# Kernel tuning notes

Measured on AMD Instinct MI355X. Metric: run time of the kernel, lower is better.

Reference implementation:

```python
import jax, jax.numpy as jnp
import numpy as np

N_NODES = 100000
N_EDGES = 3200000
N_GRAPHS = 1000
C = 11   # atomic features
D = 4    # bond features
BN_EPS = 1e-5


def setup_inputs() -> dict:
    key = jax.random.key(0)
    ks = jax.random.split(key, 20)
    inp = {
        "x": jax.random.normal(ks[0], (N_NODES, C), dtype=jnp.float32),
        "edge_index": jax.random.randint(ks[1], (2, N_EDGES), 0, N_NODES),
        "edge_attr": jax.random.uniform(ks[2], (N_EDGES, D), dtype=jnp.float32),
        "batch": jnp.sort(jax.random.randint(ks[3], (N_NODES,), 0, N_GRAPHS)),
    }
    s = 0.3
    # CGConv layer 1 params: lin_f, lin_s take z=[x_i, x_j, e] of dim 2C+D
    inp["Wf1"] = jax.random.normal(ks[4], (2 * C + D, C), dtype=jnp.float32) * s
    inp["bf1"] = jnp.zeros((C,), jnp.float32)
    inp["Ws1"] = jax.random.normal(ks[5], (2 * C + D, C), dtype=jnp.float32) * s
    inp["bs1"] = jnp.zeros((C,), jnp.float32)
    inp["gamma1"] = jnp.ones((C,), jnp.float32)
    inp["beta1"] = jnp.zeros((C,), jnp.float32)
    # CGConv layer 2
    inp["Wf2"] = jax.random.normal(ks[6], (2 * C + D, C), dtype=jnp.float32) * s
    inp["bf2"] = jnp.zeros((C,), jnp.float32)
    inp["Ws2"] = jax.random.normal(ks[7], (2 * C + D, C), dtype=jnp.float32) * s
    inp["bs2"] = jnp.zeros((C,), jnp.float32)
    inp["gamma2"] = jnp.ones((C,), jnp.float32)
    inp["beta2"] = jnp.zeros((C,), jnp.float32)
    # MLP head
    inp["W_fc1"] = jax.random.normal(ks[8], (C, 5), dtype=jnp.float32) * s
    inp["b_fc1"] = jnp.zeros((5,), jnp.float32)
    inp["W_fc2"] = jax.random.normal(ks[9], (5, 1), dtype=jnp.float32) * s
    inp["b_fc2"] = jnp.zeros((1,), jnp.float32)
    return inp


def _cgconv(x, src, dst, e, Wf, bf, Ws, bs, gamma, beta):
    # z = [x_i, x_j, e_ij] per edge; message = sigmoid(lin_f(z)) * softplus(lin_s(z))
    z = jnp.concatenate([x[dst], x[src], e], axis=-1)          # [E, 2C+D]
    msg = jax.nn.sigmoid(z @ Wf + bf) * jax.nn.softplus(z @ Ws + bs)  # [E, C]
    agg = jax.ops.segment_sum(msg, dst, num_segments=N_NODES)  # [N, C]
    # BatchNorm1d (training-mode: batch statistics over nodes)
    mu = jnp.mean(agg, axis=0)
    var = jnp.var(agg, axis=0)
    agg = (agg - mu) * jax.lax.rsqrt(var + BN_EPS) * gamma + beta
    return x + agg  # residual


def reference(x, edge_index, edge_attr, batch,
              Wf1, bf1, Ws1, bs1, gamma1, beta1,
              Wf2, bf2, Ws2, bs2, gamma2, beta2,
              W_fc1, b_fc1, W_fc2, b_fc2):
    src, dst = edge_index[0], edge_index[1]
    h = _cgconv(x, src, dst, edge_attr, Wf1, bf1, Ws1, bs1, gamma1, beta1)
    h = _cgconv(h, src, dst, edge_attr, Wf2, bf2, Ws2, bs2, gamma2, beta2)
    # global mean pool per graph
    sums = jax.ops.segment_sum(h, batch, num_segments=N_GRAPHS)        # [G, C]
    cnts = jax.ops.segment_sum(jnp.ones((h.shape[0],), h.dtype), batch,
                               num_segments=N_GRAPHS)
    pooled = sums / jnp.maximum(cnts, 1.0)[:, None]
    out = jax.nn.softplus(pooled @ W_fc1 + b_fc1)
    out = out @ W_fc2 + b_fc2                                          # [G, 1]
    return out
```

## Files before the change

### kernel.cpp

```cpp
#include <hip/hip_runtime.h>
#include <math.h>

#define N_NODES 100000
#define N_EDGES 3200000
#define N_GRAPHS 1000
#define C 11
#define D 4
#define AST 12
#define XWST 24
#define BN_EPS 1e-5f
#define LOG2E 1.44269504088896f
#define LN2   0.69314718055994f
#define QSCALE (1.0f/65535.0f)

#define BSHIFT 8
#define BNODES 256
#define NB ((N_NODES + BNODES - 1) / BNODES)
#define CAP 8704
#define EPB 8192
#define PBLK ((N_EDGES + EPB - 1) / EPB)
#define SB 64
#define PST 48

__device__ __forceinline__ float fast_sigmoid(float x) {
    float e = exp2f(-LOG2E * x);
    return __builtin_amdgcn_rcpf(1.0f + e);
}
__device__ __forceinline__ float fast_softplus(float x) {
    float e = exp2f(LOG2E * x);
    float l = log2f(1.0f + e) * LN2;
    return (x > 20.0f) ? x : l;
}

__global__ void __launch_bounds__(256) partition_kernel(
    const int* __restrict__ ei, const float4* __restrict__ ea,
    int* __restrict__ bcur, uint3* __restrict__ grp)
{
    __shared__ int lh[NB];
    __shared__ int lbase[NB];
    for (int i = threadIdx.x; i < NB; i += 256) lh[i] = 0;
    __syncthreads();
    int e0 = blockIdx.x * EPB;
    for (int r = 0; r < EPB; r += 256) {
        int e = e0 + r + threadIdx.x;
        if (e < N_EDGES) atomicAdd(&lh[ei[N_EDGES + e] >> BSHIFT], 1);
    }
    __syncthreads();
    for (int b = threadIdx.x; b < NB; b += 256) {
        lbase[b] = atomicAdd(&bcur[b], lh[b]);
        lh[b] = 0;
    }
    __syncthreads();
    for (int r = 0; r < EPB; r += 256) {
        int e = e0 + r + threadIdx.x;
        if (e < N_EDGES) {
            int d = ei[N_EDGES + e];
            int s = ei[e];
            float4 v = ea[e];
            unsigned q0 = (unsigned)(v.x * 65535.0f + 0.5f);
            unsigned q1 = (unsigned)(v.y * 65535.0f + 0.5f);
            unsigned q2 = (unsigned)(v.z * 65535.0f + 0.5f);
            unsigned q3 = (unsigned)(v.w * 65535.0f + 0.5f);
            int b = d >> BSHIFT;
            int ofs = lbase[b] + atomicAdd(&lh[b], 1);
            grp[(size_t)b * CAP + ofs] =
                make_uint3((unsigned)s | ((unsigned)(d & 255) << 17),
                           q0 | (q1 << 16), q2 | (q3 << 16));
        }
    }
}

__global__ void __launch_bounds__(512) bscan_kernel(
    const int* __restrict__ bcur, int* __restrict__ bexcl, int* __restrict__ off)
{
    __shared__ int wsum[8];
    int t = threadIdx.x;
    int lane = t & 63, w = t >> 6;
    int v = (t < NB) ? bcur[t] : 0;
    int incl = v;
    #pragma unroll
    for (int d = 1; d < 64; d <<= 1) {
        int u = __shfl_up(incl, d);
        if (lane >= d) incl += u;
    }
    if (lane == 63) wsum[w] = incl;
    __syncthreads();
    if (w == 0) {
        int x = (lane < 8) ? wsum[lane] : 0;
        #pragma unroll
        for (int d = 1; d < 8; d <<= 1) {
            int u = __shfl_up(x, d);
            if (lane >= d) x += u;
        }
        if (lane < 8) wsum[lane] = x;
    }
    __syncthreads();
    int excl = incl - v + (w > 0 ? wsum[w - 1] : 0);
    if (t < NB) bexcl[t] = excl;
    if (t == 0) { bexcl[NB] = N_EDGES; off[N_NODES] = N_EDGES; }
}

__global__ void __launch_bounds__(256) finalize_kernel(
    const uint3* __restrict__ grp, const int* __restrict__ bcur,
    const int* __restrict__ bexcl,
    int* __restrict__ off, uint3* __restrict__ rec)
{
    __shared__ int lcnt[BNODES];
    __shared__ int lexcl[BNODES];
    __shared__ int wsum[4];
    int b = blockIdx.x;
    int cnt = min(bcur[b], CAP);
    int base = bexcl[b];
    const uint3* g = grp + (size_t)b * CAP;
    int t = threadIdx.x;
    lcnt[t] = 0;
    __syncthreads();
    for (int i = t; i < cnt; i += 256)
        atomicAdd(&lcnt[(g[i].x >> 17) & 255], 1);
    __syncthreads();
    int lane = t & 63, w = t >> 6;
    int v = lcnt[t];
    int incl = v;
    #pragma unroll
    for (int d = 1; d < 64; d <<= 1) {
        int u = __shfl_up(incl, d);
        if (lane >= d) incl += u;
    }
    if (lane == 63) wsum[w] = incl;
    __syncthreads();
    if (w == 0) {
        int x = (lane < 4) ? wsum[lane] : 0;
        #pragma unroll
        for (int d = 1; d < 4; d <<= 1) {
            int u = __shfl_up(x, d);
            if (lane >= d) x += u;
        }
        if (lane < 4) wsum[lane] = x;
    }
    __syncthreads();
    int excl = incl - v + (w > 0 ? wsum[w - 1] : 0);
    lexcl[t] = excl;
    int n = (b << BSHIFT) + t;
    if (n < N_NODES) off[n] = base + excl;
    lcnt[t] = 0;
    __syncthreads();
    for (int i = t; i < cnt; i += 256) {
        uint3 r = g[i];
        int nl = (r.x >> 17) & 255;
        int pos = base + lexcl[nl] + atomicAdd(&lcnt[nl], 1);
        rec[pos] = make_uint3(r.x & 0x1FFFFu, r.y, r.z);
    }
}

__global__ void __launch_bounds__(256) pre_kernel(
    const float* __restrict__ xin, int stride,
    const float* __restrict__ Wf, const float* __restrict__ Ws,
    const float* __restrict__ bf, const float* __restrict__ bs,
    float* __restrict__ xwd, float* __restrict__ xws)
{
    __shared__ float sW[22 * C * 2];
    __shared__ float sbf[C], sbs[C];
    for (int i = threadIdx.x; i < 22 * C; i += blockDim.x) {
        sW[2 * i] = Wf[i];
        sW[2 * i + 1] = Ws[i];
    }
    if (threadIdx.x < C) { sbf[threadIdx.x] = bf[threadIdx.x]; sbs[threadIdx.x] = bs[threadIdx.x]; }
    __syncthreads();

    int n = blockIdx.x * blockDim.x + threadIdx.x;
    if (n >= N_NODES) return;
    float xi[C];
    #pragma unroll
    for (int j = 0; j < C; ++j) xi[j] = xin[n * stride + j];

    float od[XWST], os[XWST];
    #pragma unroll
    for (int c = 0; c < C; ++c) {
        float f = sbf[c], s = sbs[c];
        float f2 = 0.0f, s2 = 0.0f;
        #pragma unroll
        for (int j = 0; j < C; ++j) {
            f  = fmaf(xi[j], sW[2 * (j * C + c)], f);
            s  = fmaf(xi[j], sW[2 * (j * C + c) + 1], s);
            f2 = fmaf(xi[j], sW[2 * ((C + j) * C + c)], f2);
            s2 = fmaf(xi[j], sW[2 * ((C + j) * C + c) + 1], s2);
        }
        od[2 * c] = f; od[2 * c + 1] = s;
        os[2 * c] = f2; os[2 * c + 1] = s2;
    }
    od[22] = 0.0f; od[23] = 0.0f; os[22] = 0.0f; os[23] = 0.0f;
    float4* pd = (float4*)(xwd + (size_t)n * XWST);
    float4* ps = (float4*)(xws + (size_t)n * XWST);
    #pragma unroll
    for (int i = 0; i < 6; ++i) {
        pd[i] = make_float4(od[4 * i], od[4 * i + 1], od[4 * i + 2], od[4 * i + 3]);
        ps[i] = make_float4(os[4 * i], os[4 * i + 1], os[4 * i + 2], os[4 * i + 3]);
    }
}

__global__ void __launch_bounds__(256) conv_kernel(
    const uint3* __restrict__ rec, const int* __restrict__ off,
    const float* __restrict__ xwd, const float* __restrict__ xws,
    const float* __restrict__ Wf, const float* __restrict__ Ws,
    float* __restrict__ agg)
{
    int tid = blockIdx.x * blockDim.x + threadIdx.x;
    int n = tid >> 3;
    int t = tid & 7;
    if (n >= N_NODES) return;

    float weaf[44], weas[44];
    {
        const float2* pf = (const float2*)(Wf + 22 * C);
        const float2* ps = (const float2*)(Ws + 22 * C);
        #pragma unroll
        for (int i = 0; i < 22; ++i) {
            float2 a = pf[i], b = ps[i];
            weaf[2 * i] = a.x; weaf[2 * i + 1] = a.y;
            weas[2 * i] = b.x; weas[2 * i + 1] = b.y;
        }
    }
    float based[XWST];
    {
        const float4* pd = (const float4*)(xwd + (size_t)n * XWST);
        #pragma unroll
        for (int i = 0; i < 6; ++i) {
            float4 a = pd[i];
            based[4 * i] = a.x; based[4 * i + 1] = a.y;
            based[4 * i + 2] = a.z; based[4 * i + 3] = a.w;
        }
    }

    float acc[C];
    #pragma unroll
    for (int c = 0; c < C; ++c) acc[c] = 0.0f;

    int e1 = off[n + 1];
    for (int k = off[n] + t; k < e1; k += 8) {
        uint3 r = rec[k];
        int src = (int)r.x;
        float ea0 = (float)(r.y & 0xFFFFu) * QSCALE;
        float ea1 = (float)(r.y >> 16) * QSCALE;
        float ea2 = (float)(r.z & 0xFFFFu) * QSCALE;
        float ea3 = (float)(r.z >> 16) * QSCALE;
        float xsr[XWST];
        {
            const float4* px = (const float4*)(xws + (size_t)src * XWST);
            #pragma unroll
            for (int i = 0; i < 6; ++i) {
                float4 a = px[i];
                xsr[4 * i] = a.x; xsr[4 * i + 1] = a.y;
                xsr[4 * i + 2] = a.z; xsr[4 * i + 3] = a.w;
            }
        }
        #pragma unroll
        for (int c = 0; c < C; ++c) {
            float f = based[2 * c] + xsr[2 * c];
            float s = based[2 * c + 1] + xsr[2 * c + 1];
            f = fmaf(ea0, weaf[c], f);         s = fmaf(ea0, weas[c], s);
            f = fmaf(ea1, weaf[C + c], f);     s = fmaf(ea1, weas[C + c], s);
            f = fmaf(ea2, weaf[2 * C + c], f); s = fmaf(ea2, weas[2 * C + c], s);
            f = fmaf(ea3, weaf[3 * C + c], f); s = fmaf(ea3, weas[3 * C + c], s);
            acc[c] += fast_sigmoid(f) * fast_softplus(s);
        }
    }

    #pragma unroll
    for (int c = 0; c < C; ++c) {
        acc[c] += __shfl_xor(acc[c], 1);
        acc[c] += __shfl_xor(acc[c], 2);
        acc[c] += __shfl_xor(acc[c], 4);
    }
    if (t == 0) {
        float4* pa = (float4*)(agg + (size_t)n * AST);
        pa[0] = make_float4(acc[0], acc[1], acc[2], acc[3]);
        pa[1] = make_float4(acc[4], acc[5], acc[6], acc[7]);
        pa[2] = make_float4(acc[8], acc[9], acc[10], 0.0f);
    }
}

__global__ void __launch_bounds__(256) bn_stats_kernel(
    const float* __restrict__ agg, float* __restrict__ pstats )
{
    float s[C], q[C];
    #pragma unroll
    for (int c = 0; c < C; ++c) { s[c] = 0.0f; q[c] = 0.0f; }
    for (int n = blockIdx.x * 256 + threadIdx.x; n < N_NODES; n += SB * 256) {
        const float4* pa = (const float4*)(agg + (size_t)n * AST);
        float4 a0 = pa[0], a1 = pa[1], a2 = pa[2];
        float v[C] = {a0.x, a0.y, a0.z, a0.w, a1.x, a1.y, a1.z, a1.w,
                      a2.x, a2.y, a2.z};
        #pragma unroll
        for (int c = 0; c < C; ++c) { s[c] += v[c]; q[c] += v[c] * v[c]; }
    }
    #pragma unroll
    for (int c = 0; c < C; ++c) {
        #pragma unroll
        for (int o = 32; o > 0; o >>= 1) {
            s[c] += __shfl_down(s[c], o);
            q[c] += __shfl_down(q[c], o);
        }
    }
    __shared__ float ls[2 * C + 2];
    if (threadIdx.x < 2 * C + 2) ls[threadIdx.x] = 0.0f;
    __syncthreads();
    if ((threadIdx.x & 63) == 0) {
        #pragma unroll
        for (int c = 0; c < C; ++c) {
            atomicAdd(&ls[2 * c], s[c]);
            atomicAdd(&ls[2 * c + 1], q[c]);
        }
    }
    __syncthreads();
    if (threadIdx.x < 2 * C)
        pstats[blockIdx.x * PST + threadIdx.x] = ls[threadIdx.x];
}

__device__ __forceinline__ void reduce_stats(
    const float* __restrict__ pstats, float* smu, float* srs)
{
    if (threadIdx.x < C) {
        double sum = 0.0, sq = 0.0;
        for (int b = 0; b < SB; ++b) {
            sum += (double)pstats[b * PST + 2 * threadIdx.x];
            sq  += (double)pstats[b * PST + 2 * threadIdx.x + 1];
        }
        double mu = sum / (double)N_NODES;
        double var = sq / (double)N_NODES - mu * mu;
        smu[threadIdx.x] = (float)mu;
        srs[threadIdx.x] = (float)(1.0 / sqrt(var + (double)BN_EPS));
    }
}

__global__ void __launch_bounds__(256) bnpre_kernel(
    const float* __restrict__ xin, const float* __restrict__ agg,
    const float* __restrict__ pstats,
    const float* __restrict__ gamma, const float* __restrict__ beta,
    const float* __restrict__ Wf, const float* __restrict__ Ws,
    const float* __restrict__ bf, const float* __restrict__ bs,
    float* __restrict__ hout, float* __restrict__ xwd, float* __restrict__ xws)
{
    __shared__ float sW[22 * C * 2];
    __shared__ float sbf[C], sbs[C];
    __shared__ float smu[C], srs[C], sg[C], sb[C];
    for (int i = threadIdx.x; i < 22 * C; i += blockDim.x) {
        sW[2 * i] = Wf[i];
        sW[2 * i + 1] = Ws[i];
    }
    reduce_stats(pstats, smu, srs);
    if (threadIdx.x < C) {
        sbf[threadIdx.x] = bf[threadIdx.x];
        sbs[threadIdx.x] = bs[threadIdx.x];
        sg[threadIdx.x] = gamma[threadIdx.x];
        sb[threadIdx.x] = beta[threadIdx.x];
    }
    __syncthreads();

    int n = blockIdx.x * blockDim.x + threadIdx.x;
    if (n >= N_NODES) return;

    float hv[C];
    #pragma unroll
    for (int c = 0; c < C; ++c) {
        float a = agg[n * AST + c];
        hv[c] = xin[n * C + c] + (a - smu[c]) * srs[c] * sg[c] + sb[c];
    }
    {
        float4* ph = (float4*)(hout + (size_t)n * AST);
        ph[0] = make_float4(hv[0], hv[1], hv[2], hv[3]);
        ph[1] = make_float4(hv[4], hv[5], hv[6], hv[7]);
        ph[2] = make_float4(hv[8], hv[9], hv[10], 0.0f);
    }

    float od[XWST], os[XWST];
    #pragma unroll
    for (int c = 0; c < C; ++c) {
        float f = sbf[c], s = sbs[c];
        float f2 = 0.0f, s2 = 0.0f;
        #pragma unroll
        for (int j = 0; j < C; ++j) {
            f  = fmaf(hv[j], sW[2 * (j * C + c)], f);
            s  = fmaf(hv[j], sW[2 * (j * C + c) + 1], s);
            f2 = fmaf(hv[j], sW[2 * ((C + j) * C + c)], f2);
            s2 = fmaf(hv[j], sW[2 * ((C + j) * C + c) + 1], s2);
        }
        od[2 * c] = f; od[2 * c + 1] = s;
        os[2 * c] = f2; os[2 * c + 1] = s2;
    }
    od[22] = 0.0f; od[23] = 0.0f; os[22] = 0.0f; os[23] = 0.0f;
    float4* pd = (float4*)(xwd + (size_t)n * XWST);
    float4* ps = (float4*)(xws + (size_t)n * XWST);
    #pragma unroll
    for (int i = 0; i < 6; ++i) {
        pd[i] = make_float4(od[4 * i], od[4 * i + 1], od[4 * i + 2], od[4 * i + 3]);
        ps[i] = make_float4(os[4 * i], os[4 * i + 1], os[4 * i + 2], os[4 * i + 3]);
    }
}

__global__ void __launch_bounds__(256) bn_apply_kernel(
    const float* __restrict__ hin, const float* __restrict__ agg,
    const float* __restrict__ pstats,
    const float* __restrict__ gamma, const float* __restrict__ beta,
    float* __restrict__ hout)
{
    __shared__ float smu[C], srs[C], sg[C], sb[C];
    reduce_stats(pstats, smu, srs);
    if (threadIdx.x < C) {
        sg[threadIdx.x] = gamma[threadIdx.x];
        sb[threadIdx.x] = beta[threadIdx.x];
    }
    __syncthreads();
    int n = blockIdx.x * blockDim.x + threadIdx.x;
    if (n >= N_NODES) return;
    float hv[C];
    #pragma unroll
    for (int c = 0; c < C; ++c) {
        float a = agg[n * AST + c];
        hv[c] = hin[n * AST + c] + (a - smu[c]) * srs[c] * sg[c] + sb[c];
    }
    float4* ph = (float4*)(hout + (size_t)n * AST);
    ph[0] = make_float4(hv[0], hv[1], hv[2], hv[3]);
    ph[1] = make_float4(hv[4], hv[5], hv[6], hv[7]);
    ph[2] = make_float4(hv[8], hv[9], hv[10], 0.0f);
}

__global__ void __launch_bounds__(256) pool_kernel(
    const float* __restrict__ h, const int* __restrict__ batch,
    float* __restrict__ gsum, float* __restrict__ gcnt)
{
    const int PER = 8;
    int t = blockIdx.x * blockDim.x + threadIdx.x;
    int start = t * PER;
    if (start >= N_NODES) return;
    int end = min(start + PER, N_NODES);

    int g = batch[start];
    float acc[C];
    #pragma unroll
    for (int c = 0; c < C; ++c) acc[c] = 0.0f;
    float cnt = 0.0f;
    for (int n = start; n < end; ++n) {
        int gn = batch[n];
        if (gn != g) {
            #pragma unroll
            for (int c = 0; c < C; ++c) atomicAdd(&gsum[g * C + c], acc[c]);
            atomicAdd(&gcnt[g], cnt);
            g = gn;
            #pragma unroll
            for (int c = 0; c < C; ++c) acc[c] = 0.0f;
            cnt = 0.0f;
        }
        #pragma unroll
        for (int c = 0; c < C; ++c) acc[c] += h[n * AST + c];
        cnt += 1.0f;
    }
    #pragma unroll
    for (int c = 0; c < C; ++c) atomicAdd(&gsum[g * C + c], acc[c]);
    atomicAdd(&gcnt[g], cnt);
}

__global__ void __launch_bounds__(256) head_kernel(
    const float* __restrict__ gsum, const float* __restrict__ gcnt,
    const float* __restrict__ W1, const float* __restrict__ b1,
    const float* __restrict__ W2, const float* __restrict__ b2,
    float* __restrict__ out)
{
    int g = blockIdx.x * blockDim.x + threadIdx.x;
    if (g >= N_GRAPHS) return;
    float cnt = fmaxf(gcnt[g], 1.0f);
    float p[C];
    #pragma unroll
    for (int c = 0; c < C; ++c) p[c] = gsum[g * C + c] / cnt;
    float acc = b2[0];
    #pragma unroll
    for (int j = 0; j < 5; ++j) {
        float t = b1[j];
        #pragma unroll
        for (int c = 0; c < C; ++c) t = fmaf(p[c], W1[c * 5 + j], t);
        acc = fmaf(fast_softplus(t), W2[j], acc);
    }
    out[g] = acc;
}

extern "C" void kernel_launch(void* const* d_in, const int* in_sizes, int n_in,
                              void* d_out, int out_size, void* d_ws, size_t ws_size,
                              hipStream_t stream) {
    const float* x   = (const float*)d_in[0];
    const int*   ei  = (const int*)d_in[1];
    const float* ea  = (const float*)d_in[2];
    const int*   bat = (const int*)d_in[3];
    const float* Wf1 = (const float*)d_in[4];
    const float* bf1 = (const float*)d_in[5];
    const float* Ws1 = (const float*)d_in[6];
    const float* bs1 = (const float*)d_in[7];
    const float* g1  = (const float*)d_in[8];
    const float* be1 = (const float*)d_in[9];
    const float* Wf2 = (const float*)d_in[10];
    const float* bf2 = (const float*)d_in[11];
    const float* Ws2 = (const float*)d_in[12];
    const float* bs2 = (const float*)d_in[13];
    const float* g2  = (const float*)d_in[14];
    const float* be2 = (const float*)d_in[15];
    const float* W_fc1 = (const float*)d_in[16];
    const float* b_fc1 = (const float*)d_in[17];
    const float* W_fc2 = (const float*)d_in[18];
    const float* b_fc2 = (const float*)d_in[19];
    float* out = (float*)d_out;

    char* ws = (char*)d_ws;
    size_t o = 0;
    size_t zz0 = o;
    int*    bcur   = (int*)(ws + o);    o += (size_t)NB * 4;
    float*  gsum   = (float*)(ws + o);  o += (size_t)N_GRAPHS * C * 4;
    float*  gcnt   = (float*)(ws + o);  o += (size_t)N_GRAPHS * 4;
    size_t zsize = o - zz0;
    int*    bexcl  = (int*)(ws + o);    o += (size_t)(NB + 1) * 4;
    int*    off    = (int*)(ws + o);    o += (size_t)(N_NODES + 1) * 4;
    o = (o + 255) & ~(size_t)255;
    float*  pst1   = (float*)(ws + o);  o += (size_t)SB * PST * 4;
    float*  pst2   = (float*)(ws + o);  o += (size_t)SB * PST * 4;
    o = (o + 255) & ~(size_t)255;
    uint3*  grp    = (uint3*)(ws + o);  o += (size_t)NB * CAP * 12;
    o = (o + 255) & ~(size_t)255;
    uint3*  rec    = (uint3*)(ws + o);  o += (size_t)N_EDGES * 12;
    o = (o + 255) & ~(size_t)255;
    float*  xwd    = (float*)(ws + o);  o += (size_t)N_NODES * XWST * 4;
    float*  xws    = (float*)(ws + o);  o += (size_t)N_NODES * XWST * 4;
    float*  agg    = (float*)(ws + o);  o += (size_t)N_NODES * AST * 4;
    float*  h1     = (float*)(ws + o);  o += (size_t)N_NODES * AST * 4;
    float*  h2     = xwd;

    const int cblocks = (N_NODES * 8 + 255) / 256;
    const int nblocks = (N_NODES + 255) / 256;

    hipMemsetAsync(ws + zz0, 0, zsize, stream);

    partition_kernel<<<PBLK, 256, 0, stream>>>(ei, (const float4*)ea, bcur, grp);
    bscan_kernel<<<1, 512, 0, stream>>>(bcur, bexcl, off);
    finalize_kernel<<<NB, 256, 0, stream>>>(grp, bcur, bexcl, off, rec);

    pre_kernel<<<nblocks, 256, 0, stream>>>(x, C, Wf1, Ws1, bf1, bs1, xwd, xws);
    conv_kernel<<<cblocks, 256, 0, stream>>>(rec, off, xwd, xws, Wf1, Ws1, agg);
    bn_stats_kernel<<<SB, 256, 0, stream>>>(agg, pst1);
    bnpre_kernel<<<nblocks, 256, 0, stream>>>(x, agg, pst1, g1, be1,
                                              Wf2, Ws2, bf2, bs2, h1, xwd, xws);

    conv_kernel<<<cblocks, 256, 0, stream>>>(rec, off, xwd, xws, Wf2, Ws2, agg);
    bn_stats_kernel<<<SB, 256, 0, stream>>>(agg, pst2);
    bn_apply_kernel<<<nblocks, 256, 0, stream>>>(h1, agg, pst2, g2, be2, h2);

    pool_kernel<<<(N_NODES / 8 + 255) / 256, 256, 0, stream>>>(h2, bat, gsum, gcnt);
    head_kernel<<<(N_GRAPHS + 255) / 256, 256, 0, stream>>>(gsum, gcnt, W_fc1, b_fc1,
                                                            W_fc2, b_fc2, out);
}
```

Before: 335.5 us.

## Drop per-node CSR sort; aggregate bucketed edges with shared-memory atomics

Removes the bucket scan and finalize kernels that built a per-node sorted edge list. The conv kernel now processes each 256-node bucket directly from the partitioned buffer, keeping destination features in shared memory and accumulating messages with LDS float atomics before writing them out. This saves a full pass over the 3.2M edge records and two launches. In exchange it adds atomic contention in shared memory, launches only about 391 blocks for the conv step, and makes the float summation order nondeterministic. The partition block size is also halved.

```diff
diff --git a/kernel.cpp b/kernel.cpp
--- a/kernel.cpp
+++ b/kernel.cpp
@@ -17,7 +17,7 @@
 #define BNODES 256
 #define NB ((N_NODES + BNODES - 1) / BNODES)
 #define CAP 8704
-#define EPB 8192
+#define EPB 4096
 #define PBLK ((N_EDGES + EPB - 1) / EPB)
 #define SB 64
 #define PST 48
@@ -70,88 +70,6 @@
     }
 }
 
-__global__ void __launch_bounds__(512) bscan_kernel(
-    const int* __restrict__ bcur, int* __restrict__ bexcl, int* __restrict__ off)
-{
-    __shared__ int wsum[8];
-    int t = threadIdx.x;
-    int lane = t & 63, w = t >> 6;
-    int v = (t < NB) ? bcur[t] : 0;
-    int incl = v;
-    #pragma unroll
-    for (int d = 1; d < 64; d <<= 1) {
-        int u = __shfl_up(incl, d);
-        if (lane >= d) incl += u;
-    }
-    if (lane == 63) wsum[w] = incl;
-    __syncthreads();
-    if (w == 0) {
-        int x = (lane < 8) ? wsum[lane] : 0;
-        #pragma unroll
-        for (int d = 1; d < 8; d <<= 1) {
-            int u = __shfl_up(x, d);
-            if (lane >= d) x += u;
-        }
-        if (lane < 8) wsum[lane] = x;
-    }
-    __syncthreads();
-    int excl = incl - v + (w > 0 ? wsum[w - 1] : 0);
-    if (t < NB) bexcl[t] = excl;
-    if (t == 0) { bexcl[NB] = N_EDGES; off[N_NODES] = N_EDGES; }
-}
-
-__global__ void __launch_bounds__(256) finalize_kernel(
-    const uint3* __restrict__ grp, const int* __restrict__ bcur,
-    const int* __restrict__ bexcl,
-    int* __restrict__ off, uint3* __restrict__ rec)
-{
-    __shared__ int lcnt[BNODES];
-    __shared__ int lexcl[BNODES];
-    __shared__ int wsum[4];
-    int b = blockIdx.x;
-    int cnt = min(bcur[b], CAP);
-    int base = bexcl[b];
-    const uint3* g = grp + (size_t)b * CAP;
-    int t = threadIdx.x;
-    lcnt[t] = 0;
-    __syncthreads();
-    for (int i = t; i < cnt; i += 256)
-        atomicAdd(&lcnt[(g[i].x >> 17) & 255], 1);
-    __syncthreads();
-    int lane = t & 63, w = t >> 6;
-    int v = lcnt[t];
-    int incl = v;
-    #pragma unroll
-    for (int d = 1; d < 64; d <<= 1) {
-        int u = __shfl_up(incl, d);
-        if (lane >= d) incl += u;
-    }
-    if (lane == 63) wsum[w] = incl;
-    __syncthreads();
-    if (w == 0) {
-        int x = (lane < 4) ? wsum[lane] : 0;
-        #pragma unroll
-        for (int d = 1; d < 4; d <<= 1) {
-            int u = __shfl_up(x, d);
-            if (lane >= d) x += u;
-        }
-        if (lane < 4) wsum[lane] = x;
-    }
-    __syncthreads();
-    int excl = incl - v + (w > 0 ? wsum[w - 1] : 0);
-    lexcl[t] = excl;
-    int n = (b << BSHIFT) + t;
-    if (n < N_NODES) off[n] = base + excl;
-    lcnt[t] = 0;
-    __syncthreads();
-    for (int i = t; i < cnt; i += 256) {
-        uint3 r = g[i];
-        int nl = (r.x >> 17) & 255;
-        int pos = base + lexcl[nl] + atomicAdd(&lcnt[nl], 1);
-        rec[pos] = make_uint3(r.x & 0x1FFFFu, r.y, r.z);
-    }
-}
-
 __global__ void __launch_bounds__(256) pre_kernel(
     const float* __restrict__ xin, int stride,
     const float* __restrict__ Wf, const float* __restrict__ Ws,
@@ -199,46 +117,45 @@
 }
 
 __global__ void __launch_bounds__(256) conv_kernel(
-    const uint3* __restrict__ rec, const int* __restrict__ off,
+    const uint3* __restrict__ grp, const int* __restrict__ bcur,
     const float* __restrict__ xwd, const float* __restrict__ xws,
     const float* __restrict__ Wf, const float* __restrict__ Ws,
     float* __restrict__ agg)
 {
-    int tid = blockIdx.x * blockDim.x + threadIdx.x;
-    int n = tid >> 3;
-    int t = tid & 7;
-    if (n >= N_NODES) return;
-
-    float weaf[44], weas[44];
+    __shared__ float sbased[BNODES * XWST];
+    __shared__ float sacc[BNODES * AST];
+    int b = blockIdx.x;
+    int t = threadIdx.x;
+    int n0 = b << BSHIFT;
+    int nrows = min(BNODES, N_NODES - n0);
+
+    {
+        const float4* s4 = (const float4*)(xwd + (size_t)n0 * XWST);
+        float4* d4 = (float4*)sbased;
+        int total4 = nrows * (XWST / 4);
+        for (int i = t; i < total4; i += 256) d4[i] = s4[i];
+    }
+    for (int i = t; i < BNODES * AST; i += 256) sacc[i] = 0.0f;
+
+    float wea[88];
     {
         const float2* pf = (const float2*)(Wf + 22 * C);
         const float2* ps = (const float2*)(Ws + 22 * C);
         #pragma unroll
         for (int i = 0; i < 22; ++i) {
-            float2 a = pf[i], b = ps[i];
-            weaf[2 * i] = a.x; weaf[2 * i + 1] = a.y;
-            weas[2 * i] = b.x; weas[2 * i + 1] = b.y;
-        }
-    }
-    float based[XWST];
-    {
-        const float4* pd = (const float4*)(xwd + (size_t)n * XWST);
-        #pragma unroll
-        for (int i = 0; i < 6; ++i) {
-            float4 a = pd[i];
-            based[4 * i] = a.x; based[4 * i + 1] = a.y;
-            based[4 * i + 2] = a.z; based[4 * i + 3] = a.w;
-        }
-    }
-
-    float acc[C];
-    #pragma unroll
-    for (int c = 0; c < C; ++c) acc[c] = 0.0f;
-
-    int e1 = off[n + 1];
-    for (int k = off[n] + t; k < e1; k += 8) {
-        uint3 r = rec[k];
-        int src = (int)r.x;
+            float2 a = pf[i], v = ps[i];
+            wea[4 * i + 0] = a.x; wea[4 * i + 1] = v.x;
+            wea[4 * i + 2] = a.y; wea[4 * i + 3] = v.y;
+        }
+    }
+    __syncthreads();
+
+    int cnt = min(bcur[b], CAP);
+    const uint3* g = grp + (size_t)b * CAP;
+    for (int i = t; i < cnt; i += 256) {
+        uint3 r = g[i];
+        int src = r.x & 0x1FFFF;
+        int nl  = (r.x >> 17) & 255;
         float ea0 = (float)(r.y & 0xFFFFu) * QSCALE;
         float ea1 = (float)(r.y >> 16) * QSCALE;
         float ea2 = (float)(r.z & 0xFFFFu) * QSCALE;
@@ -247,35 +164,32 @@
         {
             const float4* px = (const float4*)(xws + (size_t)src * XWST);
             #pragma unroll
-            for (int i = 0; i < 6; ++i) {
-                float4 a = px[i];
-                xsr[4 * i] = a.x; xsr[4 * i + 1] = a.y;
-                xsr[4 * i + 2] = a.z; xsr[4 * i + 3] = a.w;
+            for (int j = 0; j < 6; ++j) {
+                float4 a = px[j];
+                xsr[4 * j] = a.x; xsr[4 * j + 1] = a.y;
+                xsr[4 * j + 2] = a.z; xsr[4 * j + 3] = a.w;
             }
         }
+        const float* bas = &sbased[nl * XWST];
         #pragma unroll
         for (int c = 0; c < C; ++c) {
-            float f = based[2 * c] + xsr[2 * c];
-            float s = based[2 * c + 1] + xsr[2 * c + 1];
-            f = fmaf(ea0, weaf[c], f);         s = fmaf(ea0, weas[c], s);
-            f = fmaf(ea1, weaf[C + c], f);     s = fmaf(ea1, weas[C + c], s);
-            f = fmaf(ea2, weaf[2 * C + c], f); s = fmaf(ea2, weas[2 * C + c], s);
-            f = fmaf(ea3, weaf[3 * C + c], f); s = fmaf(ea3, weas[3 * C + c], s);
-            acc[c] += fast_sigmoid(f) * fast_softplus(s);
-        }
-    }
-
-    #pragma unroll
-    for (int c = 0; c < C; ++c) {
-        acc[c] += __shfl_xor(acc[c], 1);
-        acc[c] += __shfl_xor(acc[c], 2);
-        acc[c] += __shfl_xor(acc[c], 4);
-    }
-    if (t == 0) {
-        float4* pa = (float4*)(agg + (size_t)n * AST);
-        pa[0] = make_float4(acc[0], acc[1], acc[2], acc[3]);
-        pa[1] = make_float4(acc[4], acc[5], acc[6], acc[7]);
-        pa[2] = make_float4(acc[8], acc[9], acc[10], 0.0f);
+            float f = bas[2 * c]     + xsr[2 * c];
+            float s = bas[2 * c + 1] + xsr[2 * c + 1];
+            f = fmaf(ea0, wea[2 * c], f);              s = fmaf(ea0, wea[2 * c + 1], s);
+            f = fmaf(ea1, wea[2 * (11 + c)], f);       s = fmaf(ea1, wea[2 * (11 + c) + 1], s);
+            f = fmaf(ea2, wea[2 * (22 + c)], f);       s = fmaf(ea2, wea[2 * (22 + c) + 1], s);
+            f = fmaf(ea3, wea[2 * (33 + c)], f);       s = fmaf(ea3, wea[2 * (33 + c) + 1], s);
+            atomicAdd(&sacc[nl * AST + c], fast_sigmoid(f) * fast_softplus(s));
+        }
+    }
+    __syncthreads();
+
+    if (t < nrows) {
+        float* a = &sacc[t * AST];
+        float4* pa = (float4*)(agg + (size_t)(n0 + t) * AST);
+        pa[0] = make_float4(a[0], a[1], a[2], a[3]);
+        pa[1] = make_float4(a[4], a[5], a[6], a[7]);
+        pa[2] = make_float4(a[8], a[9], a[10], 0.0f);
     }
 }
 
@@ -514,38 +428,31 @@
     float*  gsum   = (float*)(ws + o);  o += (size_t)N_GRAPHS * C * 4;
     float*  gcnt   = (float*)(ws + o);  o += (size_t)N_GRAPHS * 4;
     size_t zsize = o - zz0;
-    int*    bexcl  = (int*)(ws + o);    o += (size_t)(NB + 1) * 4;
-    int*    off    = (int*)(ws + o);    o += (size_t)(N_NODES + 1) * 4;
     o = (o + 255) & ~(size_t)255;
     float*  pst1   = (float*)(ws + o);  o += (size_t)SB * PST * 4;
     float*  pst2   = (float*)(ws + o);  o += (size_t)SB * PST * 4;
     o = (o + 255) & ~(size_t)255;
     uint3*  grp    = (uint3*)(ws + o);  o += (size_t)NB * CAP * 12;
     o = (o + 255) & ~(size_t)255;
-    uint3*  rec    = (uint3*)(ws + o);  o += (size_t)N_EDGES * 12;
-    o = (o + 255) & ~(size_t)255;
     float*  xwd    = (float*)(ws + o);  o += (size_t)N_NODES * XWST * 4;
     float*  xws    = (float*)(ws + o);  o += (size_t)N_NODES * XWST * 4;
     float*  agg    = (float*)(ws + o);  o += (size_t)N_NODES * AST * 4;
     float*  h1     = (float*)(ws + o);  o += (size_t)N_NODES * AST * 4;
     float*  h2     = xwd;
 
-    const int cblocks = (N_NODES * 8 + 255) / 256;
     const int nblocks = (N_NODES + 255) / 256;
 
     hipMemsetAsync(ws + zz0, 0, zsize, stream);
 
     partition_kernel<<<PBLK, 256, 0, stream>>>(ei, (const float4*)ea, bcur, grp);
-    bscan_kernel<<<1, 512, 0, stream>>>(bcur, bexcl, off);
-    finalize_kernel<<<NB, 256, 0, stream>>>(grp, bcur, bexcl, off, rec);
 
     pre_kernel<<<nblocks, 256, 0, stream>>>(x, C, Wf1, Ws1, bf1, bs1, xwd, xws);
-    conv_kernel<<<cblocks, 256, 0, stream>>>(rec, off, xwd, xws, Wf1, Ws1, agg);
+    conv_kernel<<<NB, 256, 0, stream>>>(grp, bcur, xwd, xws, Wf1, Ws1, agg);
     bn_stats_kernel<<<SB, 256, 0, stream>>>(agg, pst1);
     bnpre_kernel<<<nblocks, 256, 0, stream>>>(x, agg, pst1, g1, be1,
                                               Wf2, Ws2, bf2, bs2, h1, xwd, xws);
 
-    conv_kernel<<<cblocks, 256, 0, stream>>>(rec, off, xwd, xws, Wf2, Ws2, agg);
+    conv_kernel<<<NB, 256, 0, stream>>>(grp, bcur, xwd, xws, Wf2, Ws2, agg);
     bn_stats_kernel<<<SB, 256, 0, stream>>>(agg, pst2);
     bn_apply_kernel<<<nblocks, 256, 0, stream>>>(h1, agg, pst2, g2, be2, h2);
 
```

New measurement: 658.1 us. 96.2% more time.
